# Optimization experiments

Measured on AMD Instinct MI355X. Metric: run time of the kernel, lower is better.

## Reference

```python
import jax, jax.numpy as jnp
import numpy as np

NEG_SLOPE = 0.2

def setup_inputs() -> dict:
    key = jax.random.key(0)
    k1, k2, k3, k4, k5 = jax.random.split(key, 5)
    B, N, Fin, Fout, H = 4, 2048, 256, 128, 4
    h = jax.random.normal(k1, (B, N, Fin), dtype=jnp.float32)
    adj = jax.random.randint(k2, (N, N), 0, 2, dtype=jnp.int32)
    W_w = jax.random.normal(k3, (Fout, Fin), dtype=jnp.float32) * (1.414 / np.sqrt(Fin))
    W_b = jax.random.normal(k4, (Fout,), dtype=jnp.float32) * 0.01
    attn_w = jax.random.normal(k5, (H, 2 * Fout), dtype=jnp.float32) * (1.414 / np.sqrt(2 * Fout))
    return {"h": h, "adj": adj, "W_w": W_w, "W_b": W_b, "attn_w": attn_w}

def reference(h, adj, W_w, W_b, attn_w):
    Fout = W_w.shape[0]
    # Wh: [B, N, Fout]
    Wh = jnp.einsum('bnf,of->bno', h, W_w) + W_b
    a_left = attn_w[:, :Fout]   # [H, Fout]
    a_right = attn_w[:, Fout:]  # [H, Fout]
    e_left = jnp.einsum('bno,ho->bhn', Wh, a_left)   # [B, H, N]
    e_right = jnp.einsum('bno,ho->bhn', Wh, a_right)  # [B, H, N]
    # additive broadcast score: [B, H, N, N]
    e = e_left[:, :, :, None] + e_right[:, :, None, :]
    e = jnp.where(e > 0, e, NEG_SLOPE * e)  # LeakyReLU(0.2)
    mask = (adj == 0)[None, None, :, :]     # [1,1,N,N] broadcast over B,H
    e = jnp.where(mask, -jnp.inf, e)
    attn = jax.nn.softmax(e, axis=-1)
    attn = jnp.where(jnp.isnan(attn), 0.0, attn)
    # h_prime: [B, H, N, Fout]
    h_prime = jnp.einsum('bhij,bjo->bhio', attn, Wh)
    out = jnp.mean(h_prime, axis=1)
    return jax.nn.relu(out)
```

## Files before the change

### kernel.cpp

```cpp
#include <hip/hip_runtime.h>
#include <stdint.h>

#define BB 4
#define NN 2048
#define FIN 256
#define FOUT 128
#define NH 4
#define NEG_SLOPE 0.2f

typedef short bf16x8 __attribute__((ext_vector_type(8)));
typedef unsigned short u16x8 __attribute__((ext_vector_type(8)));
typedef float f32x4 __attribute__((ext_vector_type(4)));
typedef unsigned long long u64;

__device__ inline float b2f(unsigned short u) {
    union { unsigned int i; float f; } x; x.i = ((unsigned int)u) << 16; return x.f;
}
__device__ inline unsigned short f2b(float f) {
    union { float f; unsigned int i; } x; x.f = f;
    unsigned int r = x.i + 0x7fffu + ((x.i >> 16) & 1u);
    return (unsigned short)(r >> 16);
}
__device__ inline unsigned short f2b_fast(float f) {
    union { float f; unsigned int i; } x; x.f = f;
    return (unsigned short)((x.i + 0x8000u) >> 16);
}

__global__ __launch_bounds__(256) void k0_prep(const float* __restrict__ Ww,
                                               unsigned short* __restrict__ Whi,
                                               unsigned short* __restrict__ Wlo,
                                               const int* __restrict__ adj,
                                               u64* __restrict__ mask) {
    int bid = blockIdx.x;
    if (bid < 128) {
        int idx = bid * 256 + threadIdx.x;
        float v = Ww[idx];
        unsigned short hb = f2b(v);
        Whi[idx] = hb;
        Wlo[idx] = f2b(v - b2f(hb));
    } else {
        int row = bid - 128;
        int wave = threadIdx.x >> 6, lane = threadIdx.x & 63;
        #pragma unroll
        for (int it = 0; it < 8; ++it) {
            int w = it * 4 + wave;
            int j = w * 64 + lane;
            u64 m = __ballot(adj[(size_t)row * NN + j] != 0);
            if (lane == 0) mask[row * 32 + w] = m;
        }
    }
}

__global__ __launch_bounds__(256) void k1_wh(
    const float* __restrict__ h, const unsigned short* __restrict__ Whi,
    const unsigned short* __restrict__ Wlo, const float* __restrict__ Wb,
    const float* __restrict__ attw, unsigned short* __restrict__ WhT,
    float2* __restrict__ ELpair, float2* __restrict__ ERf) {
    __shared__ unsigned short Ahi[16][264];
    __shared__ unsigned short Alo[16][264];
    __shared__ float whs[16][132];
    int t = threadIdx.x;
    int b = blockIdx.x >> 7;
    int n0 = (blockIdx.x & 127) * 16;
    {
        int r = t >> 4, c = (t & 15) * 16;
        const float* hp = h + ((size_t)(b * NN + n0 + r)) * FIN + c;
        u16x8 hi0, hi1, lo0, lo1;
        #pragma unroll
        for (int q = 0; q < 4; ++q) {
            float4 v = *(const float4*)(hp + q * 4);
            float vv[4] = {v.x, v.y, v.z, v.w};
            #pragma unroll
            for (int e = 0; e < 4; ++e) {
                int idx = q * 4 + e;
                unsigned short hb = f2b(vv[e]);
                unsigned short lb = f2b(vv[e] - b2f(hb));
                if (idx < 8) { hi0[idx] = (short)hb; lo0[idx] = (short)lb; }
                else         { hi1[idx - 8] = (short)hb; lo1[idx - 8] = (short)lb; }
            }
        }
        *(u16x8*)&Ahi[r][c] = *(u16x8*)&hi0;
        *(u16x8*)&Ahi[r][c + 8] = *(u16x8*)&hi1;
        *(u16x8*)&Alo[r][c] = *(u16x8*)&lo0;
        *(u16x8*)&Alo[r][c + 8] = *(u16x8*)&lo1;
    }
    __syncthreads();
    int lane = t & 63, wv = t >> 6;
    int m = lane & 15, quad = lane >> 4;
    int o0 = wv * 32;
    f32x4 acc0 = {0.f, 0.f, 0.f, 0.f}, acc1 = {0.f, 0.f, 0.f, 0.f};
    const unsigned short* wh0 = Whi + (size_t)(o0 + m) * FIN;
    const unsigned short* wl0 = Wlo + (size_t)(o0 + m) * FIN;
    const unsigned short* wh1 = Whi + (size_t)(o0 + 16 + m) * FIN;
    const unsigned short* wl1 = Wlo + (size_t)(o0 + 16 + m) * FIN;
    #pragma unroll
    for (int ks = 0; ks < 8; ++ks) {
        int ko = ks * 32 + quad * 8;
        bf16x8 ahi = *(bf16x8*)&Ahi[m][ko];
        bf16x8 alo = *(bf16x8*)&Alo[m][ko];
        bf16x8 bh0 = *(const bf16x8*)(wh0 + ko);
        bf16x8 bl0 = *(const bf16x8*)(wl0 + ko);
        bf16x8 bh1 = *(const bf16x8*)(wh1 + ko);
        bf16x8 bl1 = *(const bf16x8*)(wl1 + ko);
        acc0 = __builtin_amdgcn_mfma_f32_16x16x32_bf16(ahi, bh0, acc0, 0, 0, 0);
        acc0 = __builtin_amdgcn_mfma_f32_16x16x32_bf16(ahi, bl0, acc0, 0, 0, 0);
        acc0 = __builtin_amdgcn_mfma_f32_16x16x32_bf16(alo, bh0, acc0, 0, 0, 0);
        acc1 = __builtin_amdgcn_mfma_f32_16x16x32_bf16(ahi, bh1, acc1, 0, 0, 0);
        acc1 = __builtin_amdgcn_mfma_f32_16x16x32_bf16(ahi, bl1, acc1, 0, 0, 0);
        acc1 = __builtin_amdgcn_mfma_f32_16x16x32_bf16(alo, bh1, acc1, 0, 0, 0);
    }
    float bias0 = Wb[o0 + m], bias1 = Wb[o0 + 16 + m];
    #pragma unroll
    for (int reg = 0; reg < 4; ++reg) {
        int row = quad * 4 + reg;
        whs[row][o0 + m] = acc0[reg] + bias0;
        whs[row][o0 + 16 + m] = acc1[reg] + bias1;
    }
    __syncthreads();
    {
        int o = t >> 1, half = t & 1;
        u16x8 v8;
        #pragma unroll
        for (int r = 0; r < 8; ++r) v8[r] = (short)f2b(whs[half * 8 + r][o]);
        *(u16x8*)(WhT + (size_t)(b * FOUT + o) * NN + n0 + half * 8) = v8;
    }
    {
        int outi = t >> 1, half = t & 1;
        int i = outi >> 3, d = outi & 7, hh = d & 3, side = d >> 2;
        const float* arow = attw + hh * (2 * FOUT) + side * FOUT + half * 64;
        float s = 0.f;
        #pragma unroll 8
        for (int k = 0; k < 64; ++k) s = fmaf(whs[i][half * 64 + k], arow[k], s);
        s += __shfl_xor(s, 1);
        if (half == 0) {
            float p = __expf(s), n = __expf(NEG_SLOPE * s);
            if (side == 0) {
                ELpair[(size_t)(b * NH + hh) * NN + n0 + i] = make_float2(p, n);
            } else {
                ERf[((size_t)b * NN + n0 + i) * NH + hh] = make_float2(p, n);
            }
        }
    }
}

__global__ __launch_bounds__(512, 4) void k2_fused(
    const unsigned short* __restrict__ WhT, const float2* __restrict__ ERf,
    const float2* __restrict__ ELpair, const u64* __restrict__ mask,
    float* __restrict__ out) {
    __shared__ unsigned short wt[16][264];
    __shared__ u64 mws[16][32];
    __shared__ float part[32][16][NH];
    __shared__ float elsc_s[16][8];
    int t = threadIdx.x;
    int b = blockIdx.y, i0 = blockIdx.x * 16;
    int lane = t & 63, wv = t >> 6;
    int m = lane & 15, quad = lane >> 4;

    {
        int r = t >> 5, w = t & 31;
        mws[r][w] = mask[(size_t)(i0 + r) * 32 + w];
    }
    __syncthreads();

    {
        int i = t & 15, strip = t >> 4;
        float elp[NH], eln[NH], acc[NH];
        #pragma unroll
        for (int hh = 0; hh < NH; ++hh) {
            float2 e2 = ELpair[(size_t)(b * NH + hh) * NN + i0 + i];
            elp[hh] = e2.x; eln[hh] = e2.y; acc[hh] = 0.f;
        }
        u64 mw = mws[i][strip];
        const float4* erb = (const float4*)(ERf + ((size_t)b * NN + strip * 64) * NH);
        #pragma unroll 8
        for (int jj = 0; jj < 64; ++jj) {
            float4 e0 = erb[jj * 2];
            float4 e1 = erb[jj * 2 + 1];
            bool bit = (mw >> jj) & 1ull;
            float m0 = fmaxf(elp[0] * e0.x, eln[0] * e0.y);
            float m1 = fmaxf(elp[1] * e0.z, eln[1] * e0.w);
            float m2 = fmaxf(elp[2] * e1.x, eln[2] * e1.y);
            float m3 = fmaxf(elp[3] * e1.z, eln[3] * e1.w);
            acc[0] += bit ? m0 : 0.f;
            acc[1] += bit ? m1 : 0.f;
            acc[2] += bit ? m2 : 0.f;
            acc[3] += bit ? m3 : 0.f;
        }
        #pragma unroll
        for (int hh = 0; hh < NH; ++hh) part[strip][i][hh] = acc[hh];
    }
    __syncthreads();
    if (t < 64) {
        int i = t >> 2, hh = t & 3;
        float s = 0.f;
        #pragma unroll
        for (int st = 0; st < 32; ++st) s += part[st][i][hh];
        float iv = (s > 0.f) ? 0.25f / s : 0.f;
        float2 e2 = ELpair[(size_t)(b * NH + hh) * NN + i0 + i];
        elsc_s[i][hh * 2]     = e2.x * iv;
        elsc_s[i][hh * 2 + 1] = e2.y * iv;
    }

    const unsigned short* bp = WhT + (size_t)(b * FOUT + wv * 16 + m) * NN;
    f32x4 acc = {0.f, 0.f, 0.f, 0.f};
    for (int ch = 0; ch < 8; ++ch) {
        int j0 = ch * 256;
        __syncthreads();
        bf16x8 bfr[8];
        #pragma unroll
        for (int ks = 0; ks < 8; ++ks)
            bfr[ks] = *(const bf16x8*)(bp + j0 + ks * 32 + quad * 8);
        float erp[4][4], ern[4][4];
        #pragma unroll
        for (int q = 0; q < 4; ++q) {
            int jg = j0 + q * 64 + lane;
            const float4* ef = (const float4*)(ERf + ((size_t)b * NN + jg) * NH);
            float4 e0 = ef[0], e1 = ef[1];
            erp[q][0] = e0.x; ern[q][0] = e0.y;
            erp[q][1] = e0.z; ern[q][1] = e0.w;
            erp[q][2] = e1.x; ern[q][2] = e1.y;
            erp[q][3] = e1.z; ern[q][3] = e1.w;
        }
        #pragma unroll
        for (int r = 0; r < 2; ++r) {
            int ir = wv * 2 + r;
            float4 c0 = *(float4*)&elsc_s[ir][0];
            float4 c1 = *(float4*)&elsc_s[ir][4];
            #pragma unroll
            for (int q = 0; q < 4; ++q) {
                float p = fmaxf(c0.x * erp[q][0], c0.y * ern[q][0]);
                p += fmaxf(c0.z * erp[q][1], c0.w * ern[q][1]);
                p += fmaxf(c1.x * erp[q][2], c1.y * ern[q][2]);
                p += fmaxf(c1.z * erp[q][3], c1.w * ern[q][3]);
                wt[ir][q * 64 + lane] =
                    ((mws[ir][ch * 4 + q] >> lane) & 1ull) ? f2b_fast(p) : 0;
            }
        }
        __syncthreads();
        #pragma unroll
        for (int ks = 0; ks < 8; ++ks) {
            bf16x8 a = *(bf16x8*)&wt[m][ks * 32 + quad * 8];
            acc = __builtin_amdgcn_mfma_f32_16x16x32_bf16(a, bfr[ks], acc, 0, 0, 0);
        }
    }
    #pragma unroll
    for (int reg = 0; reg < 4; ++reg) {
        int row = quad * 4 + reg;
        out[((size_t)b * NN + i0 + row) * FOUT + wv * 16 + m] =
            fmaxf(acc[reg], 0.f);
    }
}

extern "C" void kernel_launch(void* const* d_in, const int* in_sizes, int n_in,
                              void* d_out, int out_size, void* d_ws, size_t ws_size,
                              hipStream_t stream) {
    const float* h    = (const float*)d_in[0];
    const int* adj    = (const int*)d_in[1];
    const float* Ww   = (const float*)d_in[2];
    const float* Wb   = (const float*)d_in[3];
    const float* attw = (const float*)d_in[4];
    float* out = (float*)d_out;
    char* ws = (char*)d_ws;
    unsigned short* Whi = (unsigned short*)(ws);
    unsigned short* Wlo = (unsigned short*)(ws + 65536);
    unsigned short* WhT = (unsigned short*)(ws + 131072);
    float2*       ELpair = (float2*)(ws + 2228224);
    float2*       ERf    = (float2*)(ws + 2490368);
    u64*          mask   = (u64*)(ws + 2752512);

    k0_prep<<<dim3(128 + NN), dim3(256), 0, stream>>>(Ww, Whi, Wlo, adj, mask);
    k1_wh<<<dim3(BB * NN / 16), dim3(256), 0, stream>>>(h, Whi, Wlo, Wb, attw,
                                                        WhT, ELpair, ERf);
    k2_fused<<<dim3(NN / 16, BB), dim3(512), 0, stream>>>(WhT, ERf, ELpair,
                                                          mask, out);
}
```

Baseline: 149.9 us.

## Fold softmax denominators into the main loop with per-head MFMA accumulators

```diff
diff --git a/kernel.cpp b/kernel.cpp
--- a/kernel.cpp
+++ b/kernel.cpp
@@ -25,6 +25,7 @@
     union { float f; unsigned int i; } x; x.f = f;
     return (unsigned short)((x.i + 0x8000u) >> 16);
 }
+
 
 __global__ __launch_bounds__(256) void k0_prep(const float* __restrict__ Ww,
                                                unsigned short* __restrict__ Whi,
@@ -147,10 +148,10 @@
     const unsigned short* __restrict__ WhT, const float2* __restrict__ ERf,
     const float2* __restrict__ ELpair, const u64* __restrict__ mask,
     float* __restrict__ out) {
-    __shared__ unsigned short wt[16][264];
+    __shared__ unsigned short wt[NH][16][264];
     __shared__ u64 mws[16][32];
-    __shared__ float part[32][16][NH];
-    __shared__ float elsc_s[16][8];
+    __shared__ float el_s[16][8];
+    __shared__ float S_s[16][NH];
     int t = threadIdx.x;
     int b = blockIdx.y, i0 = blockIdx.x * 16;
     int lane = t & 63, wv = t >> 6;
@@ -160,49 +161,26 @@
         int r = t >> 5, w = t & 31;
         mws[r][w] = mask[(size_t)(i0 + r) * 32 + w];
     }
-    __syncthreads();
-
-    {
-        int i = t & 15, strip = t >> 4;
-        float elp[NH], eln[NH], acc[NH];
-        #pragma unroll
-        for (int hh = 0; hh < NH; ++hh) {
-            float2 e2 = ELpair[(size_t)(b * NH + hh) * NN + i0 + i];
-            elp[hh] = e2.x; eln[hh] = e2.y; acc[hh] = 0.f;
-        }
-        u64 mw = mws[i][strip];
-        const float4* erb = (const float4*)(ERf + ((size_t)b * NN + strip * 64) * NH);
-        #pragma unroll 8
-        for (int jj = 0; jj < 64; ++jj) {
-            float4 e0 = erb[jj * 2];
-            float4 e1 = erb[jj * 2 + 1];
-            bool bit = (mw >> jj) & 1ull;
-            float m0 = fmaxf(elp[0] * e0.x, eln[0] * e0.y);
-            float m1 = fmaxf(elp[1] * e0.z, eln[1] * e0.w);
-            float m2 = fmaxf(elp[2] * e1.x, eln[2] * e1.y);
-            float m3 = fmaxf(elp[3] * e1.z, eln[3] * e1.w);
-            acc[0] += bit ? m0 : 0.f;
-            acc[1] += bit ? m1 : 0.f;
-            acc[2] += bit ? m2 : 0.f;
-            acc[3] += bit ? m3 : 0.f;
-        }
-        #pragma unroll
-        for (int hh = 0; hh < NH; ++hh) part[strip][i][hh] = acc[hh];
-    }
-    __syncthreads();
-    if (t < 64) {
-        int i = t >> 2, hh = t & 3;
-        float s = 0.f;
-        #pragma unroll
-        for (int st = 0; st < 32; ++st) s += part[st][i][hh];
-        float iv = (s > 0.f) ? 0.25f / s : 0.f;
+    if (t < 128) {
+        int i = t >> 3, d = t & 7, hh = d >> 1, s = d & 1;
         float2 e2 = ELpair[(size_t)(b * NH + hh) * NN + i0 + i];
-        elsc_s[i][hh * 2]     = e2.x * iv;
-        elsc_s[i][hh * 2 + 1] = e2.y * iv;
-    }
+        el_s[i][hh * 2 + s] = s ? e2.y : e2.x;
+    }
+    __syncthreads();
+
+    int ir0 = wv * 2, ir1 = ir0 + 1;
+    float4 c00 = *(float4*)&el_s[ir0][0];
+    float4 c01 = *(float4*)&el_s[ir0][4];
+    float4 c10 = *(float4*)&el_s[ir1][0];
+    float4 c11 = *(float4*)&el_s[ir1][4];
 
     const unsigned short* bp = WhT + (size_t)(b * FOUT + wv * 16 + m) * NN;
-    f32x4 acc = {0.f, 0.f, 0.f, 0.f};
+    f32x4 acc[NH];
+    #pragma unroll
+    for (int hh = 0; hh < NH; ++hh) acc[hh] = (f32x4){0.f, 0.f, 0.f, 0.f};
+    float sp0[NH] = {0.f, 0.f, 0.f, 0.f};
+    float sp1[NH] = {0.f, 0.f, 0.f, 0.f};
+
     for (int ch = 0; ch < 8; ++ch) {
         int j0 = ch * 256;
         __syncthreads();
@@ -210,44 +188,84 @@
         #pragma unroll
         for (int ks = 0; ks < 8; ++ks)
             bfr[ks] = *(const bf16x8*)(bp + j0 + ks * 32 + quad * 8);
-        float erp[4][4], ern[4][4];
         #pragma unroll
         for (int q = 0; q < 4; ++q) {
             int jg = j0 + q * 64 + lane;
             const float4* ef = (const float4*)(ERf + ((size_t)b * NN + jg) * NH);
             float4 e0 = ef[0], e1 = ef[1];
-            erp[q][0] = e0.x; ern[q][0] = e0.y;
-            erp[q][1] = e0.z; ern[q][1] = e0.w;
-            erp[q][2] = e1.x; ern[q][2] = e1.y;
-            erp[q][3] = e1.z; ern[q][3] = e1.w;
-        }
-        #pragma unroll
-        for (int r = 0; r < 2; ++r) {
-            int ir = wv * 2 + r;
-            float4 c0 = *(float4*)&elsc_s[ir][0];
-            float4 c1 = *(float4*)&elsc_s[ir][4];
+            bool bit0 = (mws[ir0][ch * 4 + q] >> lane) & 1ull;
+            bool bit1 = (mws[ir1][ch * 4 + q] >> lane) & 1ull;
+            {
+                float w0 = fmaxf(c00.x * e0.x, c00.y * e0.y);
+                float w1 = fmaxf(c00.z * e0.z, c00.w * e0.w);
+                float w2 = fmaxf(c01.x * e1.x, c01.y * e1.y);
+                float w3 = fmaxf(c01.z * e1.z, c01.w * e1.w);
+                unsigned short u0 = bit0 ? f2b_fast(w0) : 0;
+                unsigned short u1 = bit0 ? f2b_fast(w1) : 0;
+                unsigned short u2 = bit0 ? f2b_fast(w2) : 0;
+                unsigned short u3 = bit0 ? f2b_fast(w3) : 0;
+                wt[0][ir0][q * 64 + lane] = u0;
+                wt[1][ir0][q * 64 + lane] = u1;
+                wt[2][ir0][q * 64 + lane] = u2;
+                wt[3][ir0][q * 64 + lane] = u3;
+                sp0[0] += b2f(u0); sp0[1] += b2f(u1);
+                sp0[2] += b2f(u2); sp0[3] += b2f(u3);
+            }
+            {
+                float w0 = fmaxf(c10.x * e0.x, c10.y * e0.y);
+                float w1 = fmaxf(c10.z * e0.z, c10.w * e0.w);
+                float w2 = fmaxf(c11.x * e1.x, c11.y * e1.y);
+                float w3 = fmaxf(c11.z * e1.z, c11.w * e1.w);
+                unsigned short u0 = bit1 ? f2b_fast(w0) : 0;
+                unsigned short u1 = bit1 ? f2b_fast(w1) : 0;
+                unsigned short u2 = bit1 ? f2b_fast(w2) : 0;
+                unsigned short u3 = bit1 ? f2b_fast(w3) : 0;
+                wt[0][ir1][q * 64 + lane] = u0;
+                wt[1][ir1][q * 64 + lane] = u1;
+                wt[2][ir1][q * 64 + lane] = u2;
+                wt[3][ir1][q * 64 + lane] = u3;
+                sp1[0] += b2f(u0); sp1[1] += b2f(u1);
+                sp1[2] += b2f(u2); sp1[3] += b2f(u3);
+            }
+        }
+        __syncthreads();
+        #pragma unroll
+        for (int ks = 0; ks < 8; ++ks) {
             #pragma unroll
-            for (int q = 0; q < 4; ++q) {
-                float p = fmaxf(c0.x * erp[q][0], c0.y * ern[q][0]);
-                p += fmaxf(c0.z * erp[q][1], c0.w * ern[q][1]);
-                p += fmaxf(c1.x * erp[q][2], c1.y * ern[q][2]);
-                p += fmaxf(c1.z * erp[q][3], c1.w * ern[q][3]);
-                wt[ir][q * 64 + lane] =
-                    ((mws[ir][ch * 4 + q] >> lane) & 1ull) ? f2b_fast(p) : 0;
-            }
-        }
-        __syncthreads();
-        #pragma unroll
-        for (int ks = 0; ks < 8; ++ks) {
-            bf16x8 a = *(bf16x8*)&wt[m][ks * 32 + quad * 8];
-            acc = __builtin_amdgcn_mfma_f32_16x16x32_bf16(a, bfr[ks], acc, 0, 0, 0);
-        }
-    }
+            for (int hh = 0; hh < NH; ++hh) {
+                bf16x8 a = *(bf16x8*)&wt[hh][m][ks * 32 + quad * 8];
+                acc[hh] = __builtin_amdgcn_mfma_f32_16x16x32_bf16(a, bfr[ks], acc[hh], 0, 0, 0);
+            }
+        }
+    }
+    #pragma unroll
+    for (int hh = 0; hh < NH; ++hh) {
+        #pragma unroll
+        for (int s = 1; s < 64; s <<= 1) {
+            sp0[hh] += __shfl_xor(sp0[hh], s);
+            sp1[hh] += __shfl_xor(sp1[hh], s);
+        }
+    }
+    if (lane == 0) {
+        #pragma unroll
+        for (int hh = 0; hh < NH; ++hh) {
+            S_s[ir0][hh] = sp0[hh];
+            S_s[ir1][hh] = sp1[hh];
+        }
+    }
+    __syncthreads();
     #pragma unroll
     for (int reg = 0; reg < 4; ++reg) {
         int row = quad * 4 + reg;
+        float v = 0.f;
+        #pragma unroll
+        for (int hh = 0; hh < NH; ++hh) {
+            float S = S_s[row][hh];
+            float iv = (S > 0.f) ? 1.f / S : 0.f;
+            v += acc[hh][reg] * iv;
+        }
         out[((size_t)b * NN + i0 + row) * FOUT + wv * 16 + m] =
-            fmaxf(acc[reg], 0.f);
+            fmaxf(0.25f * v, 0.f);
     }
 }
 
```

Measured after the change: 144.8 us. 3.4% less time.

## Restructure attention kernel: per-head MFMA with ones-matrix row sums and register-built A fragments

Applied to the files above, without the earlier changes.

```diff
diff --git a/kernel.cpp b/kernel.cpp
--- a/kernel.cpp
+++ b/kernel.cpp
@@ -25,6 +25,7 @@
     union { float f; unsigned int i; } x; x.f = f;
     return (unsigned short)((x.i + 0x8000u) >> 16);
 }
+
 
 __global__ __launch_bounds__(256) void k0_prep(const float* __restrict__ Ww,
                                                unsigned short* __restrict__ Whi,
@@ -143,111 +144,149 @@
     }
 }
 
-__global__ __launch_bounds__(512, 4) void k2_fused(
+__global__ __launch_bounds__(512, 2) void k2_reg(
     const unsigned short* __restrict__ WhT, const float2* __restrict__ ERf,
     const float2* __restrict__ ELpair, const u64* __restrict__ mask,
     float* __restrict__ out) {
-    __shared__ unsigned short wt[16][264];
-    __shared__ u64 mws[16][32];
-    __shared__ float part[32][16][NH];
-    __shared__ float elsc_s[16][8];
+    __shared__ char smem[65536 + 8448 + 1024];
+    float4* erf4 = (float4*)smem;
+    u64* mlds = (u64*)(smem + 65536);
+    float* sred = (float*)(smem + 65536 + 8448);
     int t = threadIdx.x;
-    int b = blockIdx.y, i0 = blockIdx.x * 16;
+    int b = blockIdx.y, i0 = blockIdx.x * 32;
     int lane = t & 63, wv = t >> 6;
     int m = lane & 15, quad = lane >> 4;
-
-    {
-        int r = t >> 5, w = t & 31;
-        mws[r][w] = mask[(size_t)(i0 + r) * 32 + w];
-    }
-    __syncthreads();
-
-    {
-        int i = t & 15, strip = t >> 4;
-        float elp[NH], eln[NH], acc[NH];
-        #pragma unroll
-        for (int hh = 0; hh < NH; ++hh) {
-            float2 e2 = ELpair[(size_t)(b * NH + hh) * NN + i0 + i];
-            elp[hh] = e2.x; eln[hh] = e2.y; acc[hh] = 0.f;
-        }
-        u64 mw = mws[i][strip];
-        const float4* erb = (const float4*)(ERf + ((size_t)b * NN + strip * 64) * NH);
-        #pragma unroll 8
-        for (int jj = 0; jj < 64; ++jj) {
-            float4 e0 = erb[jj * 2];
-            float4 e1 = erb[jj * 2 + 1];
-            bool bit = (mw >> jj) & 1ull;
-            float m0 = fmaxf(elp[0] * e0.x, eln[0] * e0.y);
-            float m1 = fmaxf(elp[1] * e0.z, eln[1] * e0.w);
-            float m2 = fmaxf(elp[2] * e1.x, eln[2] * e1.y);
-            float m3 = fmaxf(elp[3] * e1.z, eln[3] * e1.w);
-            acc[0] += bit ? m0 : 0.f;
-            acc[1] += bit ? m1 : 0.f;
-            acc[2] += bit ? m2 : 0.f;
-            acc[3] += bit ? m3 : 0.f;
-        }
-        #pragma unroll
-        for (int hh = 0; hh < NH; ++hh) part[strip][i][hh] = acc[hh];
-    }
-    __syncthreads();
-    if (t < 64) {
-        int i = t >> 2, hh = t & 3;
-        float s = 0.f;
-        #pragma unroll
-        for (int st = 0; st < 32; ++st) s += part[st][i][hh];
-        float iv = (s > 0.f) ? 0.25f / s : 0.f;
-        float2 e2 = ELpair[(size_t)(b * NH + hh) * NN + i0 + i];
-        elsc_s[i][hh * 2]     = e2.x * iv;
-        elsc_s[i][hh * 2 + 1] = e2.y * iv;
-    }
-
-    const unsigned short* bp = WhT + (size_t)(b * FOUT + wv * 16 + m) * NN;
-    f32x4 acc = {0.f, 0.f, 0.f, 0.f};
-    for (int ch = 0; ch < 8; ++ch) {
-        int j0 = ch * 256;
-        __syncthreads();
-        bf16x8 bfr[8];
-        #pragma unroll
-        for (int ks = 0; ks < 8; ++ks)
-            bfr[ks] = *(const bf16x8*)(bp + j0 + ks * 32 + quad * 8);
-        float erp[4][4], ern[4][4];
-        #pragma unroll
-        for (int q = 0; q < 4; ++q) {
-            int jg = j0 + q * 64 + lane;
-            const float4* ef = (const float4*)(ERf + ((size_t)b * NN + jg) * NH);
-            float4 e0 = ef[0], e1 = ef[1];
-            erp[q][0] = e0.x; ern[q][0] = e0.y;
-            erp[q][1] = e0.z; ern[q][1] = e0.w;
-            erp[q][2] = e1.x; ern[q][2] = e1.y;
-            erp[q][3] = e1.z; ern[q][3] = e1.w;
-        }
-        #pragma unroll
-        for (int r = 0; r < 2; ++r) {
-            int ir = wv * 2 + r;
-            float4 c0 = *(float4*)&elsc_s[ir][0];
-            float4 c1 = *(float4*)&elsc_s[ir][4];
-            #pragma unroll
-            for (int q = 0; q < 4; ++q) {
-                float p = fmaxf(c0.x * erp[q][0], c0.y * ern[q][0]);
-                p += fmaxf(c0.z * erp[q][1], c0.w * ern[q][1]);
-                p += fmaxf(c1.x * erp[q][2], c1.y * ern[q][2]);
-                p += fmaxf(c1.z * erp[q][3], c1.w * ern[q][3]);
-                wt[ir][q * 64 + lane] =
-                    ((mws[ir][ch * 4 + q] >> lane) & 1ull) ? f2b_fast(p) : 0;
+    int isub = wv & 1, oq = (wv >> 1) & 1, kp = wv >> 2;
+
+    {
+        const float4* src = (const float4*)(ERf + (size_t)b * NN * NH);
+        #pragma unroll
+        for (int i = 0; i < 8; ++i) erf4[t + i * 512] = src[t + i * 512];
+    }
+    {
+        #pragma unroll
+        for (int i = 0; i < 2; ++i) {
+            int idx = t + i * 512;
+            int r = idx >> 5, w = idx & 31;
+            mlds[r * 33 + w] = mask[(size_t)(i0 + r) * 32 + w];
+        }
+    }
+    int irow = i0 + isub * 16 + m;
+    float elp[NH], eln[NH];
+    #pragma unroll
+    for (int hh = 0; hh < NH; ++hh) {
+        float2 e2 = ELpair[(size_t)(b * NH + hh) * NN + irow];
+        elp[hh] = e2.x; eln[hh] = e2.y;
+    }
+    __syncthreads();
+
+    bf16x8 ones;
+    #pragma unroll
+    for (int e = 0; e < 8; ++e) ones[e] = (short)0x3F80;
+
+    const unsigned short* bp0 = WhT + (size_t)(b * FOUT + oq * 64 +  0 + m) * NN;
+    const unsigned short* bp1 = WhT + (size_t)(b * FOUT + oq * 64 + 16 + m) * NN;
+    const unsigned short* bp2 = WhT + (size_t)(b * FOUT + oq * 64 + 32 + m) * NN;
+    const unsigned short* bp3 = WhT + (size_t)(b * FOUT + oq * 64 + 48 + m) * NN;
+
+    f32x4 acc[4][4];
+    f32x4 sacc[4];
+    #pragma unroll
+    for (int f = 0; f < 4; ++f)
+        #pragma unroll
+        for (int hh = 0; hh < NH; ++hh) acc[f][hh] = (f32x4){0.f, 0.f, 0.f, 0.f};
+    #pragma unroll
+    for (int hh = 0; hh < NH; ++hh) sacc[hh] = (f32x4){0.f, 0.f, 0.f, 0.f};
+
+    int mr = isub * 16 + m;
+
+    for (int it = 0; it < 32; ++it) {
+        int ks = (it << 1) | kp;
+        int jb = ks * 32 + quad * 8;
+        bf16x8 bfr0 = *(const bf16x8*)(bp0 + jb);
+        bf16x8 bfr1 = *(const bf16x8*)(bp1 + jb);
+        bf16x8 bfr2 = *(const bf16x8*)(bp2 + jb);
+        bf16x8 bfr3 = *(const bf16x8*)(bp3 + jb);
+        u64 w64 = mlds[mr * 33 + (ks >> 1)];
+        unsigned mb = (unsigned)(w64 >> (((ks & 1) << 5) + (quad << 3))) & 0xFFu;
+        bf16x8 af0, af1, af2, af3;
+        #pragma unroll
+        for (int e = 0; e < 8; ++e) {
+            float4 e0 = erf4[(jb + e) * 2];
+            float4 e1 = erf4[(jb + e) * 2 + 1];
+            bool bit = (mb >> e) & 1u;
+            float w0 = fmaxf(elp[0] * e0.x, eln[0] * e0.y);
+            float w1 = fmaxf(elp[1] * e0.z, eln[1] * e0.w);
+            float w2 = fmaxf(elp[2] * e1.x, eln[2] * e1.y);
+            float w3 = fmaxf(elp[3] * e1.z, eln[3] * e1.w);
+            af0[e] = bit ? (short)f2b_fast(w0) : (short)0;
+            af1[e] = bit ? (short)f2b_fast(w1) : (short)0;
+            af2[e] = bit ? (short)f2b_fast(w2) : (short)0;
+            af3[e] = bit ? (short)f2b_fast(w3) : (short)0;
+        }
+        sacc[0] = __builtin_amdgcn_mfma_f32_16x16x32_bf16(af0, ones, sacc[0], 0, 0, 0);
+        sacc[1] = __builtin_amdgcn_mfma_f32_16x16x32_bf16(af1, ones, sacc[1], 0, 0, 0);
+        sacc[2] = __builtin_amdgcn_mfma_f32_16x16x32_bf16(af2, ones, sacc[2], 0, 0, 0);
+        sacc[3] = __builtin_amdgcn_mfma_f32_16x16x32_bf16(af3, ones, sacc[3], 0, 0, 0);
+        acc[0][0] = __builtin_amdgcn_mfma_f32_16x16x32_bf16(af0, bfr0, acc[0][0], 0, 0, 0);
+        acc[0][1] = __builtin_amdgcn_mfma_f32_16x16x32_bf16(af1, bfr0, acc[0][1], 0, 0, 0);
+        acc[0][2] = __builtin_amdgcn_mfma_f32_16x16x32_bf16(af2, bfr0, acc[0][2], 0, 0, 0);
+        acc[0][3] = __builtin_amdgcn_mfma_f32_16x16x32_bf16(af3, bfr0, acc[0][3], 0, 0, 0);
+        acc[1][0] = __builtin_amdgcn_mfma_f32_16x16x32_bf16(af0, bfr1, acc[1][0], 0, 0, 0);
+        acc[1][1] = __builtin_amdgcn_mfma_f32_16x16x32_bf16(af1, bfr1, acc[1][1], 0, 0, 0);
+        acc[1][2] = __builtin_amdgcn_mfma_f32_16x16x32_bf16(af2, bfr1, acc[1][2], 0, 0, 0);
+        acc[1][3] = __builtin_amdgcn_mfma_f32_16x16x32_bf16(af3, bfr1, acc[1][3], 0, 0, 0);
+        acc[2][0] = __builtin_amdgcn_mfma_f32_16x16x32_bf16(af0, bfr2, acc[2][0], 0, 0, 0);
+        acc[2][1] = __builtin_amdgcn_mfma_f32_16x16x32_bf16(af1, bfr2, acc[2][1], 0, 0, 0);
+        acc[2][2] = __builtin_amdgcn_mfma_f32_16x16x32_bf16(af2, bfr2, acc[2][2], 0, 0, 0);
+        acc[2][3] = __builtin_amdgcn_mfma_f32_16x16x32_bf16(af3, bfr2, acc[2][3], 0, 0, 0);
+        acc[3][0] = __builtin_amdgcn_mfma_f32_16x16x32_bf16(af0, bfr3, acc[3][0], 0, 0, 0);
+        acc[3][1] = __builtin_amdgcn_mfma_f32_16x16x32_bf16(af1, bfr3, acc[3][1], 0, 0, 0);
+        acc[3][2] = __builtin_amdgcn_mfma_f32_16x16x32_bf16(af2, bfr3, acc[3][2], 0, 0, 0);
+        acc[3][3] = __builtin_amdgcn_mfma_f32_16x16x32_bf16(af3, bfr3, acc[3][3], 0, 0, 0);
+    }
+    __syncthreads();
+
+    float* cred = (float*)smem;
+    int p = wv & 3;
+    if (kp == 1) {
+        #pragma unroll
+        for (int f = 0; f < 4; ++f)
+            #pragma unroll
+            for (int hh = 0; hh < NH; ++hh)
+                #pragma unroll
+                for (int r = 0; r < 4; ++r)
+                    cred[(((p * 4 + f) * 4 + hh) * 4 + r) * 64 + lane] = acc[f][hh][r];
+        if (m == 0) {
+            #pragma unroll
+            for (int hh = 0; hh < NH; ++hh)
+                #pragma unroll
+                for (int r = 0; r < 4; ++r)
+                    sred[((p * 4 + hh) * 4 + r) * 4 + quad] = sacc[hh][r];
+        }
+    }
+    __syncthreads();
+    if (kp == 0) {
+        #pragma unroll
+        for (int r = 0; r < 4; ++r) {
+            float inv[NH];
+            #pragma unroll
+            for (int hh = 0; hh < NH; ++hh) {
+                float S = sacc[hh][r] + sred[((p * 4 + hh) * 4 + r) * 4 + quad];
+                inv[hh] = (S > 0.f) ? 1.f / S : 0.f;
             }
-        }
-        __syncthreads();
-        #pragma unroll
-        for (int ks = 0; ks < 8; ++ks) {
-            bf16x8 a = *(bf16x8*)&wt[m][ks * 32 + quad * 8];
-            acc = __builtin_amdgcn_mfma_f32_16x16x32_bf16(a, bfr[ks], acc, 0, 0, 0);
-        }
-    }
-    #pragma unroll
-    for (int reg = 0; reg < 4; ++reg) {
-        int row = quad * 4 + reg;
-        out[((size_t)b * NN + i0 + row) * FOUT + wv * 16 + m] =
-            fmaxf(acc[reg], 0.f);
+            int orow = i0 + isub * 16 + quad * 4 + r;
+            #pragma unroll
+            for (int f = 0; f < 4; ++f) {
+                float v = 0.f;
+                #pragma unroll
+                for (int hh = 0; hh < NH; ++hh)
+                    v += (acc[f][hh][r] +
+                          cred[(((p * 4 + f) * 4 + hh) * 4 + r) * 64 + lane]) * inv[hh];
+                out[((size_t)b * NN + orow) * FOUT + oq * 64 + f * 16 + m] =
+                    fmaxf(0.25f * v, 0.f);
+            }
+        }
     }
 }
 
@@ -271,6 +310,6 @@
     k0_prep<<<dim3(128 + NN), dim3(256), 0, stream>>>(Ww, Whi, Wlo, adj, mask);
     k1_wh<<<dim3(BB * NN / 16), dim3(256), 0, stream>>>(h, Whi, Wlo, Wb, attw,
                                                         WhT, ELpair, ERf);
-    k2_fused<<<dim3(NN / 16, BB), dim3(512), 0, stream>>>(WhT, ERf, ELpair,
-                                                          mask, out);
-}
+    k2_reg<<<dim3(NN / 32, BB), dim3(512), 0, stream>>>(WhT, ERf, ELpair,
+                                                        mask, out);
+}
```

Result: faster. 128.5 us (-14.3%).
